# Performance work log

Hardware: AMD Instinct MI355X
Metric: run time of the kernel (lower is better)

## Reference

```python
import jax, jax.numpy as jnp
import numpy as np

POS_DIM = 3
LATENT = 128
HEADS = 4
HEAD_DIM = LATENT // HEADS
KERNEL_IN = 4 * POS_DIM - POS_DIM + 1  # q_pos,o_pos,rel,dist -> 10
N_Q = 1024
N_O = 2048
LN_EPS = 1e-5


def setup_inputs() -> dict:
    key = jax.random.key(0)
    ks = jax.random.split(key, 9)
    s = lambda fan_in: 1.0 / np.sqrt(fan_in)
    return {
        "h_obs": jax.random.normal(ks[0], (N_O, LATENT), dtype=jnp.float32),
        "pos_obs": jax.random.normal(ks[1], (N_O, POS_DIM), dtype=jnp.float32),
        "pos_query": jax.random.normal(ks[2], (N_Q, POS_DIM), dtype=jnp.float32),
        "obs_batch": jnp.zeros((N_O,), dtype=jnp.int32),
        "query_batch": jnp.zeros((N_Q,), dtype=jnp.int32),
        # kernel_mlp: Linear(10, 128) -> ReLU -> Linear(128, 4); stored as [in, out]
        "W1": jax.random.uniform(ks[3], (KERNEL_IN, LATENT), jnp.float32, -s(KERNEL_IN), s(KERNEL_IN)),
        "b1": jnp.zeros((LATENT,), jnp.float32),
        "W2": jax.random.uniform(ks[4], (LATENT, HEADS), jnp.float32, -s(LATENT), s(LATENT)),
        "b2": jnp.zeros((HEADS,), jnp.float32),
        "ln_gamma": jnp.ones((LATENT,), jnp.float32),
        "ln_beta": jnp.zeros((LATENT,), jnp.float32),
        "Wv": jax.random.uniform(ks[5], (LATENT, LATENT), jnp.float32, -s(LATENT), s(LATENT)),
        "bv": jnp.zeros((LATENT,), jnp.float32),
    }


def reference(h_obs, pos_obs, pos_query, obs_batch, query_batch,
              W1, b1, W2, b2, ln_gamma, ln_beta, Wv, bv):
    N_q, N_o = pos_query.shape[0], pos_obs.shape[0]
    # pairwise relative position encodings: [N_q, N_o, 10]
    rel = pos_query[:, None, :] - pos_obs[None, :, :]            # [N_q, N_o, P]
    dist = jnp.linalg.norm(rel, axis=-1, keepdims=True)          # [N_q, N_o, 1]
    pos_q_exp = jnp.broadcast_to(pos_query[:, None, :], rel.shape)
    pos_o_exp = jnp.broadcast_to(pos_obs[None, :, :], rel.shape)
    kernel_input = jnp.concatenate([pos_q_exp, pos_o_exp, rel, dist], axis=-1)
    # per-pair MLP score -> logits [N_q, N_o, H]
    hidden = jax.nn.relu(jnp.einsum('qok,kl->qol', kernel_input, W1) + b1)
    logits = jnp.einsum('qol,lh->qoh', hidden, W2) + b2
    # same-graph mask (softmax over N_o axis)
    batch_mask = query_batch[:, None] == obs_batch[None, :]      # [N_q, N_o]
    logits = jnp.where(batch_mask[:, :, None], logits, -jnp.inf)
    weights = jax.nn.softmax(logits, axis=1)                     # over N_o
    # value path: LayerNorm -> value_proj -> heads
    mu = jnp.mean(h_obs, axis=-1, keepdims=True)
    var = jnp.var(h_obs, axis=-1, keepdims=True)
    h_norm = (h_obs - mu) * jax.lax.rsqrt(var + LN_EPS) * ln_gamma + ln_beta
    v = (h_norm @ Wv + bv).reshape(N_o, HEADS, HEAD_DIM)         # [N_o, H, D]
    # weighted aggregation: [N_q, H, D] -> [N_q, latent]
    h_query = jnp.einsum('qoh,ohd->qhd', weights, v)
    return h_query.reshape(N_q, LATENT)
```

## Files before the change

kernel.cpp:

```cpp
#include <hip/hip_runtime.h>

#define NQ 1024
#define NO 2048
#define LAT 128
#define CHUNK 16
#define NCHUNK (NO / CHUNK)
#define LDSTR 132
#define LOG2E 1.4426950408889634f
#define NEG_BIG -3.0e38f
#define MASK_THRESH -1.0e37f
#define PART_STRIDE 136
#define SY_MAX 32

__global__ __launch_bounds__(256) void gano_value(
    const float* __restrict__ ln_g,
    const float* __restrict__ ln_b,
    const float* __restrict__ Wv,
    const float* __restrict__ bv,
    float* __restrict__ h)
{
    __shared__ float hn[LAT];
    __shared__ float red[8];
    __shared__ float part[LAT];
    const int t = threadIdx.x;
    const int o = blockIdx.x;
    const int d = t & 127;
    const int kh = t >> 7;

    const float x = h[(size_t)o*LAT + d];
    float s1 = x, s2 = x*x;
#pragma unroll
    for (int off = 32; off >= 1; off >>= 1) {
        s1 += __shfl_xor(s1, off);
        s2 += __shfl_xor(s2, off);
    }
    const int w = t >> 6;
    if ((t & 63) == 0) { red[w*2] = s1; red[w*2+1] = s2; }
    __syncthreads();
    const float S1 = red[0] + red[2];
    const float S2 = red[1] + red[3];
    const float mean = S1 * (1.0f/LAT);
    const float var  = S2 * (1.0f/LAT) - mean*mean;
    const float rstd = rsqrtf(var + 1e-5f);
    if (t < LAT)
        hn[d] = (x - mean) * rstd * ln_g[d] + ln_b[d];
    __syncthreads();

    float acc = kh ? 0.f : bv[d];
    const float* wp = Wv + (size_t)(kh*64)*LAT + d;
    const float* hp = hn + kh*64;
#pragma unroll 8
    for (int kk = 0; kk < 64; ++kk)
        acc = fmaf(hp[kk], wp[(size_t)kk*LAT], acc);
    if (kh) part[d] = acc;
    __syncthreads();
    if (!kh) h[(size_t)o*LAT + d] = acc + part[d];
}

__global__ __launch_bounds__(256) void gano_main(
    const float* __restrict__ v,
    const float* __restrict__ pos_obs,
    const float* __restrict__ pos_query,
    const int* __restrict__ obs_batch,
    const int* __restrict__ query_batch,
    const float* __restrict__ W1,
    const float* __restrict__ b1,
    const float* __restrict__ W2,
    const float* __restrict__ b2,
    float* __restrict__ ws,
    float* __restrict__ out,
    int SY)
{
    __shared__ __align__(16) float ld[CHUNK*LDSTR];
    __shared__ __align__(16) float lcq[16*LDSTR];
    __shared__ __align__(16) float lgt[16*4*CHUNK];
    __shared__ float lpos[CHUNK*3];
    __shared__ int   lob[CHUNK];

    const int tid = threadIdx.x;
    const int i  = tid & 15;
    const int qi = tid >> 4;
    const int q  = blockIdx.x * 16 + qi;
    const int d0 = i * 8;
    const int hstar = i >> 2;

#pragma unroll
    for (int t2 = 0; t2 < 2; ++t2) {
        const int idx = tid + t2*256;
        const int row = idx >> 5;
        const int g   = idx & 31;
        const int dd4 = g * 4;
        const int qq  = blockIdx.x * 16 + row;
        const float px = pos_query[qq*3+0];
        const float py = pos_query[qq*3+1];
        const float pz = pos_query[qq*3+2];
        float4 c = *(const float4*)(b1 + dd4);
        const float4 wx0 = *(const float4*)(W1 + 0*LAT + dd4);
        const float4 wx6 = *(const float4*)(W1 + 6*LAT + dd4);
        const float4 wy0 = *(const float4*)(W1 + 1*LAT + dd4);
        const float4 wy6 = *(const float4*)(W1 + 7*LAT + dd4);
        const float4 wz0 = *(const float4*)(W1 + 2*LAT + dd4);
        const float4 wz6 = *(const float4*)(W1 + 8*LAT + dd4);
        c.x = fmaf(px, wx0.x+wx6.x, fmaf(py, wy0.x+wy6.x, fmaf(pz, wz0.x+wz6.x, c.x)));
        c.y = fmaf(px, wx0.y+wx6.y, fmaf(py, wy0.y+wy6.y, fmaf(pz, wz0.y+wz6.y, c.y)));
        c.z = fmaf(px, wx0.z+wx6.z, fmaf(py, wy0.z+wy6.z, fmaf(pz, wz0.z+wz6.z, c.z)));
        c.w = fmaf(px, wx0.w+wx6.w, fmaf(py, wy0.w+wy6.w, fmaf(pz, wz0.w+wz6.w, c.w)));
        *(float4*)(lcq + row*LDSTR + dd4) = c;
    }

    const float pqx = pos_query[q*3+0];
    const float pqy = pos_query[q*3+1];
    const float pqz = pos_query[q*3+2];
    const int   qb  = query_batch[q];
    const float b2l0 = b2[0]*LOG2E, b2l1 = b2[1]*LOG2E;
    const float b2l2 = b2[2]*LOG2E, b2l3 = b2[3]*LOG2E;

    float4 accA = make_float4(0.f,0.f,0.f,0.f);
    float4 accB = make_float4(0.f,0.f,0.f,0.f);
    float m = NEG_BIG, lsum = 0.f;

    for (int cb = blockIdx.y; cb < NCHUNK; cb += SY) {
        const int o0 = cb * CHUNK;
        __syncthreads();

#pragma unroll
        for (int t2 = 0; t2 < 2; ++t2) {
            const int idx = tid + t2*256;
            const int oo = idx >> 5;
            const int g  = idx & 31;
            const int d4 = g * 4;
            const float* po = pos_obs + (size_t)(o0 + oo)*3;
            const float px = po[0], py = po[1], pz = po[2];
            const float4 w3 = *(const float4*)(W1 + 3*LAT + d4);
            const float4 w4 = *(const float4*)(W1 + 4*LAT + d4);
            const float4 w5 = *(const float4*)(W1 + 5*LAT + d4);
            const float4 w6 = *(const float4*)(W1 + 6*LAT + d4);
            const float4 w7 = *(const float4*)(W1 + 7*LAT + d4);
            const float4 w8 = *(const float4*)(W1 + 8*LAT + d4);
            float4 r;
            r.x = fmaf(px, w3.x-w6.x, fmaf(py, w4.x-w7.x, pz*(w5.x-w8.x)));
            r.y = fmaf(px, w3.y-w6.y, fmaf(py, w4.y-w7.y, pz*(w5.y-w8.y)));
            r.z = fmaf(px, w3.z-w6.z, fmaf(py, w4.z-w7.z, pz*(w5.z-w8.z)));
            r.w = fmaf(px, w3.w-w6.w, fmaf(py, w4.w-w7.w, pz*(w5.w-w8.w)));
            *(float4*)(ld + oo*LDSTR + d4) = r;
        }
        for (int idx = tid; idx < CHUNK*3; idx += 256) lpos[idx] = pos_obs[o0*3 + idx];
        for (int idx = tid; idx < CHUNK;   idx += 256) lob[idx]  = obs_batch[o0 + idx];
        __syncthreads();

        {
            const int oc = i;
            const float dx = pqx - lpos[oc*3+0];
            const float dy = pqy - lpos[oc*3+1];
            const float dz = pqz - lpos[oc*3+2];
            const float dist = sqrtf(dx*dx + dy*dy + dz*dz);
            const int mb = (lob[oc] == qb);

            float lg0 = 0.f, lg1 = 0.f, lg2 = 0.f, lg3 = 0.f;
            const float* ldr = ld + oc*LDSTR;
            const float* lcr = lcq + qi*LDSTR;
#pragma unroll 4
            for (int j = 0; j < 32; ++j) {
                const float4 dd = *(const float4*)(ldr + j*4);
                const float4 cc = *(const float4*)(lcr + j*4);
                const float4 wd = *(const float4*)(W1 + 9*LAT + j*4);
                const float4 w2a = *(const float4*)(W2 + (j*4+0)*4);
                const float4 w2b = *(const float4*)(W2 + (j*4+1)*4);
                const float4 w2c = *(const float4*)(W2 + (j*4+2)*4);
                const float4 w2d = *(const float4*)(W2 + (j*4+3)*4);
                const float h0 = fmaxf(fmaf(wd.x, dist, cc.x + dd.x), 0.f);
                const float h1 = fmaxf(fmaf(wd.y, dist, cc.y + dd.y), 0.f);
                const float h2 = fmaxf(fmaf(wd.z, dist, cc.z + dd.z), 0.f);
                const float h3 = fmaxf(fmaf(wd.w, dist, cc.w + dd.w), 0.f);
                lg0 = fmaf(h0, w2a.x, lg0); lg1 = fmaf(h0, w2a.y, lg1);
                lg2 = fmaf(h0, w2a.z, lg2); lg3 = fmaf(h0, w2a.w, lg3);
                lg0 = fmaf(h1, w2b.x, lg0); lg1 = fmaf(h1, w2b.y, lg1);
                lg2 = fmaf(h1, w2b.z, lg2); lg3 = fmaf(h1, w2b.w, lg3);
                lg0 = fmaf(h2, w2c.x, lg0); lg1 = fmaf(h2, w2c.y, lg1);
                lg2 = fmaf(h2, w2c.z, lg2); lg3 = fmaf(h2, w2c.w, lg3);
                lg0 = fmaf(h3, w2d.x, lg0); lg1 = fmaf(h3, w2d.y, lg1);
                lg2 = fmaf(h3, w2d.z, lg2); lg3 = fmaf(h3, w2d.w, lg3);
            }
            const int ocr = (oc + 4*qi) & 15;
            float* lrow = lgt + (qi*4)*CHUNK + ocr;
            lrow[0*CHUNK] = mb ? fmaf(lg0, LOG2E, b2l0) : NEG_BIG;
            lrow[1*CHUNK] = mb ? fmaf(lg1, LOG2E, b2l1) : NEG_BIG;
            lrow[2*CHUNK] = mb ? fmaf(lg2, LOG2E, b2l2) : NEG_BIG;
            lrow[3*CHUNK] = mb ? fmaf(lg3, LOG2E, b2l3) : NEG_BIG;
        }
        __syncthreads();

        {
            const float* rowp = lgt + (qi*4 + hstar)*CHUNK;
            float lgv[16];
#pragma unroll
            for (int p = 0; p < 4; ++p) {
                const float4 t = *(const float4*)(rowp + ((p + qi) & 3) * 4);
                lgv[p*4+0] = t.x; lgv[p*4+1] = t.y;
                lgv[p*4+2] = t.z; lgv[p*4+3] = t.w;
            }
#pragma unroll
            for (int og = 0; og < 4; ++og) {
                const float l0 = lgv[og*4+0], l1 = lgv[og*4+1];
                const float l2 = lgv[og*4+2], l3 = lgv[og*4+3];
                const float mg = fmaxf(fmaxf(l0, l1), fmaxf(l2, l3));
                const float mn = fmaxf(m, mg);
                const float alpha = exp2f(m - mn);
                const float p0 = (l0 > MASK_THRESH) ? exp2f(l0 - mn) : 0.f;
                const float p1 = (l1 > MASK_THRESH) ? exp2f(l1 - mn) : 0.f;
                const float p2 = (l2 > MASK_THRESH) ? exp2f(l2 - mn) : 0.f;
                const float p3 = (l3 > MASK_THRESH) ? exp2f(l3 - mn) : 0.f;
                lsum = fmaf(lsum, alpha, (p0 + p1) + (p2 + p3));
                m = mn;

                const float* vp = v + (size_t)(o0 + og*4)*LAT + d0;
                const float4 v0A = *(const float4*)(vp + 0*LAT);
                const float4 v0B = *(const float4*)(vp + 0*LAT + 4);
                const float4 v1A = *(const float4*)(vp + 1*LAT);
                const float4 v1B = *(const float4*)(vp + 1*LAT + 4);
                const float4 v2A = *(const float4*)(vp + 2*LAT);
                const float4 v2B = *(const float4*)(vp + 2*LAT + 4);
                const float4 v3A = *(const float4*)(vp + 3*LAT);
                const float4 v3B = *(const float4*)(vp + 3*LAT + 4);
                accA.x = fmaf(accA.x, alpha, fmaf(p0, v0A.x, fmaf(p1, v1A.x, fmaf(p2, v2A.x, p3*v3A.x))));
                accA.y = fmaf(accA.y, alpha, fmaf(p0, v0A.y, fmaf(p1, v1A.y, fmaf(p2, v2A.y, p3*v3A.y))));
                accA.z = fmaf(accA.z, alpha, fmaf(p0, v0A.z, fmaf(p1, v1A.z, fmaf(p2, v2A.z, p3*v3A.z))));
                accA.w = fmaf(accA.w, alpha, fmaf(p0, v0A.w, fmaf(p1, v1A.w, fmaf(p2, v2A.w, p3*v3A.w))));
                accB.x = fmaf(accB.x, alpha, fmaf(p0, v0B.x, fmaf(p1, v1B.x, fmaf(p2, v2B.x, p3*v3B.x))));
                accB.y = fmaf(accB.y, alpha, fmaf(p0, v0B.y, fmaf(p1, v1B.y, fmaf(p2, v2B.y, p3*v3B.y))));
                accB.z = fmaf(accB.z, alpha, fmaf(p0, v0B.z, fmaf(p1, v1B.z, fmaf(p2, v2B.z, p3*v3B.z))));
                accB.w = fmaf(accB.w, alpha, fmaf(p0, v0B.w, fmaf(p1, v1B.w, fmaf(p2, v2B.w, p3*v3B.w))));
            }
        }
    }

    if (SY == 1) {
        const float inv = 1.0f / lsum;
        float* op = out + (size_t)q*LAT + d0;
        float4 rA, rB;
        rA.x = accA.x*inv; rA.y = accA.y*inv; rA.z = accA.z*inv; rA.w = accA.w*inv;
        rB.x = accB.x*inv; rB.y = accB.y*inv; rB.z = accB.z*inv; rB.w = accB.w*inv;
        *(float4*)op       = rA;
        *(float4*)(op + 4) = rB;
    } else {
        float* pp = ws + ((size_t)blockIdx.y * NQ + q) * PART_STRIDE;
        if ((i & 3) == 0) {
            pp[hstar]     = m;
            pp[4 + hstar] = lsum;
        }
        *(float4*)(pp + 8 + d0)     = accA;
        *(float4*)(pp + 8 + d0 + 4) = accB;
    }
}

__global__ __launch_bounds__(128) void gano_combine(
    const float* __restrict__ ws, float* __restrict__ out, int SY)
{
    const int q = blockIdx.x;
    const int l = threadIdx.x;
    const int h = l >> 5;
    float M = NEG_BIG, Ls = 0.f, A = 0.f;
    for (int s = 0; s < SY; ++s) {
        const float* pp = ws + ((size_t)s * NQ + q) * PART_STRIDE;
        const float ms = pp[h];
        const float ls = pp[4 + h];
        const float as = pp[8 + l];
        const float Mn = fmaxf(M, ms);
        const float a0 = exp2f(M - Mn);
        const float a1 = exp2f(ms - Mn);
        Ls = Ls*a0 + ls*a1;
        A  = A *a0 + as*a1;
        M = Mn;
    }
    out[(size_t)q*LAT + l] = A / Ls;
}

extern "C" void kernel_launch(void* const* d_in, const int* in_sizes, int n_in,
                              void* d_out, int out_size, void* d_ws, size_t ws_size,
                              hipStream_t stream) {
    (void)in_sizes; (void)n_in; (void)out_size;
    float*       h_obs     = (float*)d_in[0];
    const float* pos_obs   = (const float*)d_in[1];
    const float* pos_query = (const float*)d_in[2];
    const int*   obs_batch = (const int*)d_in[3];
    const int*   query_batch = (const int*)d_in[4];
    const float* W1 = (const float*)d_in[5];
    const float* b1 = (const float*)d_in[6];
    const float* W2 = (const float*)d_in[7];
    const float* b2 = (const float*)d_in[8];
    const float* ln_g = (const float*)d_in[9];
    const float* ln_b = (const float*)d_in[10];
    const float* Wv = (const float*)d_in[11];
    const float* bv = (const float*)d_in[12];
    float* ws  = (float*)d_ws;
    float* out = (float*)d_out;

    int SY = 1;
    const size_t per = (size_t)NQ * PART_STRIDE * sizeof(float);
    if (ws && ws_size >= 2*per) {
        size_t s = ws_size / per;
        SY = (int)(s < SY_MAX ? s : SY_MAX);
    }

    gano_value<<<NO, 256, 0, stream>>>(ln_g, ln_b, Wv, bv, h_obs);
    gano_main<<<dim3(NQ/16, SY), 256, 0, stream>>>(h_obs, pos_obs, pos_query,
                                                   obs_batch, query_batch,
                                                   W1, b1, W2, b2, ws, out, SY);
    if (SY > 1)
        gano_combine<<<NQ, 128, 0, stream>>>(ws, out, SY);
}
```

Baseline: 200.2 us.

## Rework value kernel, split softmax-V loop into pairs, two-pass combine

The value kernel now handles two observations per block, each with 128 threads, and uses four independent accumulators across the full K dimension. This removes the split-K partial reduction and its extra barrier. The main softmax-value loop consumes logits two at a time from a float4 read inside the loop instead of preloading 16 into registers, which lowers register pressure at the cost of more rescale steps. The combine kernel stages per-split max and sum values in shared memory, takes the global max first, then accumulates with two independent chains.

```diff
diff --git a/kernel.cpp b/kernel.cpp
--- a/kernel.cpp
+++ b/kernel.cpp
@@ -19,42 +19,42 @@
     const float* __restrict__ bv,
     float* __restrict__ h)
 {
-    __shared__ float hn[LAT];
-    __shared__ float red[8];
-    __shared__ float part[LAT];
+    __shared__ float hn[2][LAT];
+    __shared__ float red[2][4];
     const int t = threadIdx.x;
-    const int o = blockIdx.x;
+    const int o = t >> 7;
     const int d = t & 127;
-    const int kh = t >> 7;
-
-    const float x = h[(size_t)o*LAT + d];
+    const int ob = blockIdx.x * 2 + o;
+
+    const float x = h[(size_t)ob*LAT + d];
     float s1 = x, s2 = x*x;
 #pragma unroll
     for (int off = 32; off >= 1; off >>= 1) {
         s1 += __shfl_xor(s1, off);
         s2 += __shfl_xor(s2, off);
     }
-    const int w = t >> 6;
-    if ((t & 63) == 0) { red[w*2] = s1; red[w*2+1] = s2; }
+    const int wv = (t >> 6) & 1;
+    if ((t & 63) == 0) { red[o][wv*2] = s1; red[o][wv*2+1] = s2; }
     __syncthreads();
-    const float S1 = red[0] + red[2];
-    const float S2 = red[1] + red[3];
+    const float S1 = red[o][0] + red[o][2];
+    const float S2 = red[o][1] + red[o][3];
     const float mean = S1 * (1.0f/LAT);
     const float var  = S2 * (1.0f/LAT) - mean*mean;
     const float rstd = rsqrtf(var + 1e-5f);
-    if (t < LAT)
-        hn[d] = (x - mean) * rstd * ln_g[d] + ln_b[d];
+    hn[o][d] = (x - mean) * rstd * ln_g[d] + ln_b[d];
     __syncthreads();
 
-    float acc = kh ? 0.f : bv[d];
-    const float* wp = Wv + (size_t)(kh*64)*LAT + d;
-    const float* hp = hn + kh*64;
+    float a0 = bv[d], a1 = 0.f, a2 = 0.f, a3 = 0.f;
+    const float* wc = Wv + d;
+    const float* hh = hn[o];
 #pragma unroll 8
-    for (int kk = 0; kk < 64; ++kk)
-        acc = fmaf(hp[kk], wp[(size_t)kk*LAT], acc);
-    if (kh) part[d] = acc;
-    __syncthreads();
-    if (!kh) h[(size_t)o*LAT + d] = acc + part[d];
+    for (int kk = 0; kk < 32; ++kk) {
+        a0 = fmaf(hh[kk],      wc[(size_t)(kk)*LAT],      a0);
+        a1 = fmaf(hh[kk + 32], wc[(size_t)(kk + 32)*LAT], a1);
+        a2 = fmaf(hh[kk + 64], wc[(size_t)(kk + 64)*LAT], a2);
+        a3 = fmaf(hh[kk + 96], wc[(size_t)(kk + 96)*LAT], a3);
+    }
+    h[(size_t)ob*LAT + d] = (a0 + a1) + (a2 + a3);
 }
 
 __global__ __launch_bounds__(256) void gano_main(
@@ -192,44 +192,34 @@
 
         {
             const float* rowp = lgt + (qi*4 + hstar)*CHUNK;
-            float lgv[16];
-#pragma unroll
-            for (int p = 0; p < 4; ++p) {
-                const float4 t = *(const float4*)(rowp + ((p + qi) & 3) * 4);
-                lgv[p*4+0] = t.x; lgv[p*4+1] = t.y;
-                lgv[p*4+2] = t.z; lgv[p*4+3] = t.w;
-            }
 #pragma unroll
             for (int og = 0; og < 4; ++og) {
-                const float l0 = lgv[og*4+0], l1 = lgv[og*4+1];
-                const float l2 = lgv[og*4+2], l3 = lgv[og*4+3];
-                const float mg = fmaxf(fmaxf(l0, l1), fmaxf(l2, l3));
-                const float mn = fmaxf(m, mg);
-                const float alpha = exp2f(m - mn);
-                const float p0 = (l0 > MASK_THRESH) ? exp2f(l0 - mn) : 0.f;
-                const float p1 = (l1 > MASK_THRESH) ? exp2f(l1 - mn) : 0.f;
-                const float p2 = (l2 > MASK_THRESH) ? exp2f(l2 - mn) : 0.f;
-                const float p3 = (l3 > MASK_THRESH) ? exp2f(l3 - mn) : 0.f;
-                lsum = fmaf(lsum, alpha, (p0 + p1) + (p2 + p3));
-                m = mn;
-
-                const float* vp = v + (size_t)(o0 + og*4)*LAT + d0;
-                const float4 v0A = *(const float4*)(vp + 0*LAT);
-                const float4 v0B = *(const float4*)(vp + 0*LAT + 4);
-                const float4 v1A = *(const float4*)(vp + 1*LAT);
-                const float4 v1B = *(const float4*)(vp + 1*LAT + 4);
-                const float4 v2A = *(const float4*)(vp + 2*LAT);
-                const float4 v2B = *(const float4*)(vp + 2*LAT + 4);
-                const float4 v3A = *(const float4*)(vp + 3*LAT);
-                const float4 v3B = *(const float4*)(vp + 3*LAT + 4);
-                accA.x = fmaf(accA.x, alpha, fmaf(p0, v0A.x, fmaf(p1, v1A.x, fmaf(p2, v2A.x, p3*v3A.x))));
-                accA.y = fmaf(accA.y, alpha, fmaf(p0, v0A.y, fmaf(p1, v1A.y, fmaf(p2, v2A.y, p3*v3A.y))));
-                accA.z = fmaf(accA.z, alpha, fmaf(p0, v0A.z, fmaf(p1, v1A.z, fmaf(p2, v2A.z, p3*v3A.z))));
-                accA.w = fmaf(accA.w, alpha, fmaf(p0, v0A.w, fmaf(p1, v1A.w, fmaf(p2, v2A.w, p3*v3A.w))));
-                accB.x = fmaf(accB.x, alpha, fmaf(p0, v0B.x, fmaf(p1, v1B.x, fmaf(p2, v2B.x, p3*v3B.x))));
-                accB.y = fmaf(accB.y, alpha, fmaf(p0, v0B.y, fmaf(p1, v1B.y, fmaf(p2, v2B.y, p3*v3B.y))));
-                accB.z = fmaf(accB.z, alpha, fmaf(p0, v0B.z, fmaf(p1, v1B.z, fmaf(p2, v2B.z, p3*v3B.z))));
-                accB.w = fmaf(accB.w, alpha, fmaf(p0, v0B.w, fmaf(p1, v1B.w, fmaf(p2, v2B.w, p3*v3B.w))));
+                const float4 t4 = *(const float4*)(rowp + ((og + qi) & 3) * 4);
+#pragma unroll
+                for (int pr = 0; pr < 2; ++pr) {
+                    const float l0 = pr ? t4.z : t4.x;
+                    const float l1 = pr ? t4.w : t4.y;
+                    const float mn = fmaxf(m, fmaxf(l0, l1));
+                    const float alpha = exp2f(m - mn);
+                    const float p0 = (l0 > MASK_THRESH) ? exp2f(l0 - mn) : 0.f;
+                    const float p1 = (l1 > MASK_THRESH) ? exp2f(l1 - mn) : 0.f;
+                    lsum = fmaf(lsum, alpha, p0 + p1);
+                    m = mn;
+
+                    const float* vp = v + (size_t)(o0 + og*4 + pr*2)*LAT + d0;
+                    const float4 v0A = *(const float4*)(vp);
+                    const float4 v0B = *(const float4*)(vp + 4);
+                    const float4 v1A = *(const float4*)(vp + LAT);
+                    const float4 v1B = *(const float4*)(vp + LAT + 4);
+                    accA.x = fmaf(accA.x, alpha, fmaf(p0, v0A.x, p1*v1A.x));
+                    accA.y = fmaf(accA.y, alpha, fmaf(p0, v0A.y, p1*v1A.y));
+                    accA.z = fmaf(accA.z, alpha, fmaf(p0, v0A.z, p1*v1A.z));
+                    accA.w = fmaf(accA.w, alpha, fmaf(p0, v0A.w, p1*v1A.w));
+                    accB.x = fmaf(accB.x, alpha, fmaf(p0, v0B.x, p1*v1B.x));
+                    accB.y = fmaf(accB.y, alpha, fmaf(p0, v0B.y, p1*v1B.y));
+                    accB.z = fmaf(accB.z, alpha, fmaf(p0, v0B.z, p1*v1B.z));
+                    accB.w = fmaf(accB.w, alpha, fmaf(p0, v0B.w, p1*v1B.w));
+                }
             }
         }
     }
@@ -256,23 +246,39 @@
 __global__ __launch_bounds__(128) void gano_combine(
     const float* __restrict__ ws, float* __restrict__ out, int SY)
 {
+    __shared__ float lm[SY_MAX*4];
+    __shared__ float ll[SY_MAX*4];
     const int q = blockIdx.x;
     const int l = threadIdx.x;
     const int h = l >> 5;
-    float M = NEG_BIG, Ls = 0.f, A = 0.f;
-    for (int s = 0; s < SY; ++s) {
+
+    if (l < SY*4) {
+        const int s = l >> 2, hh = l & 3;
         const float* pp = ws + ((size_t)s * NQ + q) * PART_STRIDE;
-        const float ms = pp[h];
-        const float ls = pp[4 + h];
-        const float as = pp[8 + l];
-        const float Mn = fmaxf(M, ms);
-        const float a0 = exp2f(M - Mn);
-        const float a1 = exp2f(ms - Mn);
-        Ls = Ls*a0 + ls*a1;
-        A  = A *a0 + as*a1;
-        M = Mn;
-    }
-    out[(size_t)q*LAT + l] = A / Ls;
+        lm[l] = pp[hh];
+        ll[l] = pp[4 + hh];
+    }
+    __syncthreads();
+
+    float M = NEG_BIG;
+    for (int s = 0; s < SY; ++s) M = fmaxf(M, lm[s*4 + h]);
+
+    float Ls = 0.f, A0 = 0.f, A1 = 0.f;
+#pragma unroll 4
+    for (int s = 0; s + 1 < SY; s += 2) {
+        const float e0 = exp2f(lm[s*4 + h] - M);
+        const float e1 = exp2f(lm[(s+1)*4 + h] - M);
+        Ls = fmaf(ll[s*4 + h], e0, fmaf(ll[(s+1)*4 + h], e1, Ls));
+        A0 = fmaf(ws[((size_t)s     * NQ + q) * PART_STRIDE + 8 + l], e0, A0);
+        A1 = fmaf(ws[((size_t)(s+1) * NQ + q) * PART_STRIDE + 8 + l], e1, A1);
+    }
+    if (SY & 1) {
+        const int s = SY - 1;
+        const float e0 = exp2f(lm[s*4 + h] - M);
+        Ls = fmaf(ll[s*4 + h], e0, Ls);
+        A0 = fmaf(ws[((size_t)s * NQ + q) * PART_STRIDE + 8 + l], e0, A0);
+    }
+    out[(size_t)q*LAT + l] = (A0 + A1) / Ls;
 }
 
 extern "C" void kernel_launch(void* const* d_in, const int* in_sizes, int n_in,
@@ -302,7 +308,7 @@
         SY = (int)(s < SY_MAX ? s : SY_MAX);
     }
 
-    gano_value<<<NO, 256, 0, stream>>>(ln_g, ln_b, Wv, bv, h_obs);
+    gano_value<<<NO/2, 256, 0, stream>>>(ln_g, ln_b, Wv, bv, h_obs);
     gano_main<<<dim3(NQ/16, SY), 256, 0, stream>>>(h_obs, pos_obs, pos_query,
                                                    obs_batch, query_batch,
                                                    W1, b1, W2, b2, ws, out, SY);
```

Result: faster. 191.6 us (-4.3%).
